# Performance work log

Hardware: AMD Instinct MI355X
Metric: run time of the kernel (lower is better)

## Reference

```python
import jax, jax.numpy as jnp
import numpy as np

B, H = 131072, 768          # batch of CLS vectors, roberta-base hidden size
C_SIZES = (2, 3, 4, 2)      # label_dict['c'] head sizes; offsets [0,2,5,9]


def setup_inputs() -> dict:
    key = jax.random.key(0)
    ks = jax.random.split(key, 14)
    def lin(kw, kb, out_dim):
        W = jax.random.normal(kw, (out_dim, H), jnp.float32) * 0.02
        b = jax.random.normal(kb, (out_dim,), jnp.float32) * 0.02
        return W, b
    x = jax.random.normal(ks[0], (B, H), jnp.float32)
    Wa, ba = lin(ks[1], ks[2], 2)
    Wb, bb = lin(ks[3], ks[4], 4)            # label_dict['b'] - 1 = 4
    Wc1, bc1 = lin(ks[5], ks[6], C_SIZES[0])
    Wc2, bc2 = lin(ks[7], ks[8], C_SIZES[1])
    Wc3, bc3 = lin(ks[9], ks[10], C_SIZES[2])
    Wc4, bc4 = lin(ks[11], ks[12], C_SIZES[3])
    return dict(x=x, Wa=Wa, ba=ba, Wb=Wb, bb=bb,
                Wc1=Wc1, bc1=bc1, Wc2=Wc2, bc2=bc2,
                Wc3=Wc3, bc3=bc3, Wc4=Wc4, bc4=bc4)


def reference(x, Wa, ba, Wb, bb, Wc1, bc1, Wc2, bc2, Wc3, bc3, Wc4, bc4):
    # taskA head (dropout prob = 0.0 -> identity)
    out_a = x @ Wa.T + ba                          # [B, 2]
    pred_a = jnp.argmax(out_a, axis=1)             # per-sample route: 0 -> skip
    active = (pred_a != 0)[:, None]                # [B, 1]

    # taskB head, scattered into out_b[:, 1:] only for active samples
    tb = x @ Wb.T + bb                             # [B, 4]
    out_b = jnp.concatenate(
        [jnp.zeros((x.shape[0], 1), x.dtype), jnp.where(active, tb, 0.0)],
        axis=1)                                    # [B, 5]

    # taskC: taskB argmax selects one of 4 heads; outputs land at fixed
    # contiguous column offsets (get_c_offset) in out_c; inactive -> zeros.
    pred_b = jnp.argmax(tb, axis=1)                # 0..3 -> head '1'..'4'
    parts = []
    for k, (Wc, bc) in enumerate([(Wc1, bc1), (Wc2, bc2), (Wc3, bc3), (Wc4, bc4)]):
        mask = active & (pred_b == k)[:, None]     # this head routed & active
        parts.append(jnp.where(mask, x @ Wc.T + bc, 0.0))
    out_c = jnp.concatenate(parts, axis=1)         # [B, 11]

    return out_a, out_b, out_c
```

## Files before the change

### kernel.cpp

```cpp
#include <hip/hip_runtime.h>

#define HDIM 768

constexpr int KC    = 32;
constexpr int KHALF = HDIM / 2;
constexpr int NCH   = KHALF / KC;
constexpr int RPB   = 128;
constexpr int PITCH = 2 * KC + 4;

__device__ __forceinline__ void dot4(float& a, const float4 xv,
                                     const float* __restrict__ Wrow, int kb) {
    const float4 w = *(const float4*)(Wrow + kb);
    a = fmaf(xv.x, w.x, a);
    a = fmaf(xv.y, w.y, a);
    a = fmaf(xv.z, w.z, a);
    a = fmaf(xv.w, w.w, a);
}

__global__ __launch_bounds__(256, 4)
void hier_fused(const float* __restrict__ x,
                const float* __restrict__ Wa,  const float* __restrict__ ba,
                const float* __restrict__ Wb,  const float* __restrict__ bb,
                const float* __restrict__ Wc1, const float* __restrict__ bc1,
                const float* __restrict__ Wc2, const float* __restrict__ bc2,
                const float* __restrict__ Wc3, const float* __restrict__ bc3,
                const float* __restrict__ Wc4, const float* __restrict__ bc4,
                float* __restrict__ out, int B)
{
    __shared__ float xs[RPB * PITCH];

    const int t       = threadIdx.x;
    const int r       = t & (RPB - 1);
    const int kh      = t >> 7;
    const int rowBase = blockIdx.x * RPB;

    int vz;
    asm("v_mov_b32 %0, 0" : "=v"(vz));

    float acc[17];
#pragma unroll
    for (int j = 0; j < 17; ++j) acc[j] = 0.f;

    const int col4 = (t & 15) * 4;
    const int grp  = t >> 4;
    const int gOff = (col4 < KC) ? col4
                                 : (KHALF - KC + col4);

    for (int c = 0; c < NCH; ++c) {
        __syncthreads();
        const int gcol = c * KC + gOff;
#pragma unroll
        for (int i = 0; i < 8; ++i) {
            int r2  = grp + i * 16;
            int row = rowBase + r2;
            if (row >= B) row = B - 1;
            const float4 v = *(const float4*)&x[(size_t)row * HDIM + gcol];
            *(float4*)&xs[r2 * PITCH + col4] = v;
        }
        __syncthreads();

        const float* xr    = &xs[r * PITCH + kh * KC];
        const int    kbase = kh * KHALF + c * KC + vz;
#pragma unroll 2
        for (int kk = 0; kk < KC; kk += 4) {
            const float4 xv = *(const float4*)(xr + kk);
            const int kb = kbase + kk;
            dot4(acc[0],  xv, Wa,              kb);
            dot4(acc[1],  xv, Wa  +     HDIM,  kb);
            dot4(acc[2],  xv, Wb,              kb);
            dot4(acc[3],  xv, Wb  +     HDIM,  kb);
            dot4(acc[4],  xv, Wb  + 2 * HDIM,  kb);
            dot4(acc[5],  xv, Wb  + 3 * HDIM,  kb);
            dot4(acc[6],  xv, Wc1,             kb);
            dot4(acc[7],  xv, Wc1 +     HDIM,  kb);
            dot4(acc[8],  xv, Wc2,             kb);
            dot4(acc[9],  xv, Wc2 +     HDIM,  kb);
            dot4(acc[10], xv, Wc2 + 2 * HDIM,  kb);
            dot4(acc[11], xv, Wc3,             kb);
            dot4(acc[12], xv, Wc3 +     HDIM,  kb);
            dot4(acc[13], xv, Wc3 + 2 * HDIM,  kb);
            dot4(acc[14], xv, Wc3 + 3 * HDIM,  kb);
            dot4(acc[15], xv, Wc4,             kb);
            dot4(acc[16], xv, Wc4 +     HDIM,  kb);
        }
    }

    __syncthreads();
    if (kh == 1) {
#pragma unroll
        for (int j = 0; j < 17; ++j) xs[r * 18 + j] = acc[j];
    }
    __syncthreads();
    if (kh != 0) return;

#pragma unroll
    for (int j = 0; j < 17; ++j) acc[j] += xs[r * 18 + j];

    const int row = rowBase + r;
    if (row >= B) return;

    const float oa0 = acc[0] + ba[0];
    const float oa1 = acc[1] + ba[1];
    const bool active = oa1 > oa0;

    const float tb0 = acc[2] + bb[0];
    const float tb1 = acc[3] + bb[1];
    const float tb2 = acc[4] + bb[2];
    const float tb3 = acc[5] + bb[3];
    int   p = 0;
    float m = tb0;
    if (tb1 > m) { m = tb1; p = 1; }
    if (tb2 > m) { m = tb2; p = 2; }
    if (tb3 > m) { m = tb3; p = 3; }

    float* oa = out + (size_t)2 * row;
    oa[0] = oa0;
    oa[1] = oa1;

    float* ob = out + (size_t)2 * B + (size_t)5 * row;
    ob[0] = 0.f;
    ob[1] = active ? tb0 : 0.f;
    ob[2] = active ? tb1 : 0.f;
    ob[3] = active ? tb2 : 0.f;
    ob[4] = active ? tb3 : 0.f;

    const bool m0 = active && (p == 0);
    const bool m1 = active && (p == 1);
    const bool m2 = active && (p == 2);
    const bool m3 = active && (p == 3);
    float* oc = out + (size_t)7 * B + (size_t)11 * row;
    oc[0]  = m0 ? acc[6]  + bc1[0] : 0.f;
    oc[1]  = m0 ? acc[7]  + bc1[1] : 0.f;
    oc[2]  = m1 ? acc[8]  + bc2[0] : 0.f;
    oc[3]  = m1 ? acc[9]  + bc2[1] : 0.f;
    oc[4]  = m1 ? acc[10] + bc2[2] : 0.f;
    oc[5]  = m2 ? acc[11] + bc3[0] : 0.f;
    oc[6]  = m2 ? acc[12] + bc3[1] : 0.f;
    oc[7]  = m2 ? acc[13] + bc3[2] : 0.f;
    oc[8]  = m2 ? acc[14] + bc3[3] : 0.f;
    oc[9]  = m3 ? acc[15] + bc4[0] : 0.f;
    oc[10] = m3 ? acc[16] + bc4[1] : 0.f;
}

extern "C" void kernel_launch(void* const* d_in, const int* in_sizes, int n_in,
                              void* d_out, int out_size, void* d_ws, size_t ws_size,
                              hipStream_t stream) {
    const float* x   = (const float*)d_in[0];
    const float* Wa  = (const float*)d_in[1];
    const float* ba  = (const float*)d_in[2];
    const float* Wb  = (const float*)d_in[3];
    const float* bb  = (const float*)d_in[4];
    const float* Wc1 = (const float*)d_in[5];
    const float* bc1 = (const float*)d_in[6];
    const float* Wc2 = (const float*)d_in[7];
    const float* bc2 = (const float*)d_in[8];
    const float* Wc3 = (const float*)d_in[9];
    const float* bc3 = (const float*)d_in[10];
    const float* Wc4 = (const float*)d_in[11];
    const float* bc4 = (const float*)d_in[12];

    const int B  = in_sizes[0] / HDIM;
    const int nb = (B + RPB - 1) / RPB;

    hipLaunchKernelGGL(hier_fused, dim3(nb), dim3(256), 0, stream,
                       x, Wa, ba, Wb, bb, Wc1, bc1, Wc2, bc2, Wc3, bc3, Wc4, bc4,
                       (float*)d_out, B);
}
```

Before: 673.1 us.

## Register-prefetch x tiles and split K four ways over 64-row blocks

Each block now covers 64 rows with four K-splits of 16 columns per 64-wide chunk. The next chunk of x is loaded into registers while the current one is computed, then written to shared memory between barriers. Partial sums from the three extra splits are reduced through shared memory. Launch bounds rise to 6 waves per SIMD to raise occupancy and hide the latency of a memory-bound stream, at the cost of more barriers per chunk, extra reduction traffic and a tighter register budget.

Result: slower. 955.6 us (+42.0%).

```diff
diff --git a/kernel.cpp b/kernel.cpp
--- a/kernel.cpp
+++ b/kernel.cpp
@@ -2,11 +2,11 @@
 
 #define HDIM 768
 
-constexpr int KC    = 32;
-constexpr int KHALF = HDIM / 2;
-constexpr int NCH   = KHALF / KC;
-constexpr int RPB   = 128;
-constexpr int PITCH = 2 * KC + 4;
+constexpr int RPB   = 64;
+constexpr int SPL   = 4;
+constexpr int KPC   = 64;
+constexpr int NCH   = HDIM / KPC;
+constexpr int PITCH = KPC + 4;
 
 __device__ __forceinline__ void dot4(float& a, const float4 xv,
                                      const float* __restrict__ Wrow, int kb) {
@@ -17,7 +17,7 @@
     a = fmaf(xv.w, w.w, a);
 }
 
-__global__ __launch_bounds__(256, 4)
+__global__ __launch_bounds__(256, 6)
 void hier_fused(const float* __restrict__ x,
                 const float* __restrict__ Wa,  const float* __restrict__ ba,
                 const float* __restrict__ Wb,  const float* __restrict__ bb,
@@ -31,7 +31,7 @@
 
     const int t       = threadIdx.x;
     const int r       = t & (RPB - 1);
-    const int kh      = t >> 7;
+    const int s       = t >> 6;
     const int rowBase = blockIdx.x * RPB;
 
     int vz;
@@ -43,26 +43,35 @@
 
     const int col4 = (t & 15) * 4;
     const int grp  = t >> 4;
-    const int gOff = (col4 < KC) ? col4
-                                 : (KHALF - KC + col4);
 
-    for (int c = 0; c < NCH; ++c) {
-        __syncthreads();
-        const int gcol = c * KC + gOff;
+    float4 p[4];
+
+    auto fetch = [&](int c) {
 #pragma unroll
-        for (int i = 0; i < 8; ++i) {
+        for (int i = 0; i < 4; ++i) {
             int r2  = grp + i * 16;
             int row = rowBase + r2;
             if (row >= B) row = B - 1;
-            const float4 v = *(const float4*)&x[(size_t)row * HDIM + gcol];
-            *(float4*)&xs[r2 * PITCH + col4] = v;
+            p[i] = *(const float4*)&x[(size_t)row * HDIM + c * KPC + col4];
         }
-        __syncthreads();
+    };
+    auto store = [&]() {
+#pragma unroll
+        for (int i = 0; i < 4; ++i)
+            *(float4*)&xs[(grp + i * 16) * PITCH + col4] = p[i];
+    };
 
-        const float* xr    = &xs[r * PITCH + kh * KC];
-        const int    kbase = kh * KHALF + c * KC + vz;
+    fetch(0);
+    store();
+    __syncthreads();
+    fetch(1);
+
+    const float* xr = &xs[r * PITCH + s * 16];
+
+    for (int c = 0; c < NCH; ++c) {
+        const int kbase = c * KPC + s * 16 + vz;
 #pragma unroll 2
-        for (int kk = 0; kk < KC; kk += 4) {
+        for (int kk = 0; kk < 16; kk += 4) {
             const float4 xv = *(const float4*)(xr + kk);
             const int kb = kbase + kk;
             dot4(acc[0],  xv, Wa,              kb);
@@ -83,18 +92,27 @@
             dot4(acc[15], xv, Wc4,             kb);
             dot4(acc[16], xv, Wc4 +     HDIM,  kb);
         }
+        if (c + 1 < NCH) {
+            __syncthreads();
+            store();
+            __syncthreads();
+            if (c + 2 < NCH) fetch(c + 2);
+        }
     }
 
     __syncthreads();
-    if (kh == 1) {
+    if (s > 0) {
 #pragma unroll
-        for (int j = 0; j < 17; ++j) xs[r * 18 + j] = acc[j];
+        for (int j = 0; j < 17; ++j)
+            xs[((s - 1) * RPB + r) * 17 + j] = acc[j];
     }
     __syncthreads();
-    if (kh != 0) return;
-
+    if (s != 0) return;
 #pragma unroll
-    for (int j = 0; j < 17; ++j) acc[j] += xs[r * 18 + j];
+    for (int ss = 0; ss < 3; ++ss)
+#pragma unroll
+        for (int j = 0; j < 17; ++j)
+            acc[j] += xs[(ss * RPB + r) * 17 + j];
 
     const int row = rowBase + r;
     if (row >= B) return;
@@ -107,11 +125,11 @@
     const float tb1 = acc[3] + bb[1];
     const float tb2 = acc[4] + bb[2];
     const float tb3 = acc[5] + bb[3];
-    int   p = 0;
+    int   pidx = 0;
     float m = tb0;
-    if (tb1 > m) { m = tb1; p = 1; }
-    if (tb2 > m) { m = tb2; p = 2; }
-    if (tb3 > m) { m = tb3; p = 3; }
+    if (tb1 > m) { m = tb1; pidx = 1; }
+    if (tb2 > m) { m = tb2; pidx = 2; }
+    if (tb3 > m) { m = tb3; pidx = 3; }
 
     float* oa = out + (size_t)2 * row;
     oa[0] = oa0;
@@ -124,10 +142,10 @@
     ob[3] = active ? tb2 : 0.f;
     ob[4] = active ? tb3 : 0.f;
 
-    const bool m0 = active && (p == 0);
-    const bool m1 = active && (p == 1);
-    const bool m2 = active && (p == 2);
-    const bool m3 = active && (p == 3);
+    const bool m0 = active && (pidx == 0);
+    const bool m1 = active && (pidx == 1);
+    const bool m2 = active && (pidx == 2);
+    const bool m3 = active && (pidx == 3);
     float* oc = out + (size_t)7 * B + (size_t)11 * row;
     oc[0]  = m0 ? acc[6]  + bc1[0] : 0.f;
     oc[1]  = m0 ? acc[7]  + bc1[1] : 0.f;
```
